# Kernel tuning notes

Hardware: AMD Instinct MI355X
Metric: run time of the kernel (lower is better)

The kernel has to match this reference:

```python
import jax, jax.numpy as jnp
import numpy as np

EPS_NORM = 1e-8
EPS_Q = 1e-5

def rmsnorm(x, g):
    var = jnp.mean(x * x, axis=-1, keepdims=True)
    return x * jax.lax.rsqrt(var + EPS_NORM) * g

def activation_quant(x):
    # per-token int8 absmax quantization
    scale = 127.0 / jnp.clip(jnp.max(jnp.abs(x), axis=-1, keepdims=True), EPS_Q, None)
    return jnp.clip(jnp.round(x * scale), -128.0, 127.0) / scale

def weight_quant(w):
    # per-tensor ternary absmean quantization
    scale = 1.0 / jnp.clip(jnp.mean(jnp.abs(w)), EPS_Q, None)
    return jnp.clip(jnp.round(w * scale), -1.0, 1.0) / scale

def ste(x, qfn):
    # straight-through estimator: forward quantized, backward identity
    return x + jax.lax.stop_gradient(qfn(x) - x)

def bitlinear(x, w, g):
    h = rmsnorm(x, g)
    hq = ste(h, activation_quant)
    wq = ste(w, weight_quant)
    return jnp.einsum('bsh,oh->bso', hq, wq)

def setup_inputs() -> dict:
    key = jax.random.key(0)
    k1, k2, k3 = jax.random.split(key, 3)
    B, S, H = 2, 2048, 2048
    I = int(H * 4.0)  # intermediate_size = 8192
    x = jax.random.normal(k1, (B, S, H), dtype=jnp.float32)
    w_gate = jax.random.normal(k2, (2 * I, H), dtype=jnp.float32) * 0.02
    g_gate = jnp.ones((H,), dtype=jnp.float32)
    w_down = jax.random.normal(k3, (H, I), dtype=jnp.float32) * 0.02
    g_down = jnp.ones((I,), dtype=jnp.float32)
    return {"x": x, "w_gate": w_gate, "g_gate": g_gate, "w_down": w_down, "g_down": g_down}

def reference(x, w_gate, g_gate, w_down, g_down):
    y = bitlinear(x, w_gate, g_gate)        # [B,S,2I]
    gate, up = jnp.split(y, 2, axis=-1)     # each [B,S,I]
    z = bitlinear(jax.nn.silu(gate) * up, w_down, g_down)  # [B,S,H]
    return z
```

## Files before the change

### kernel.cpp

```cpp
#include <hip/hip_runtime.h>
#include <hip/hip_bf16.h>
#include <hip/hip_fp16.h>

#define DEVINL __device__ __forceinline__

typedef float f32x4 __attribute__((ext_vector_type(4)));
typedef int i32x4 __attribute__((ext_vector_type(4)));
typedef unsigned int u32x4 __attribute__((ext_vector_type(4)));
typedef unsigned int u32x2 __attribute__((ext_vector_type(2)));

typedef __attribute__((address_space(1))) void void_g;
typedef __attribute__((address_space(3))) void void_l;

DEVINL void gload16(const void* g, void* l) {
  __builtin_amdgcn_global_load_lds((void_g*)g, (void_l*)l, 16, 0, 0);
}

DEVINL float wave_sum(float v) {
  #pragma unroll
  for (int o = 32; o > 0; o >>= 1) v += __shfl_down(v, o, 64);
  return v;
}
DEVINL float wave_max(float v) {
  #pragma unroll
  for (int o = 32; o > 0; o >>= 1) v = fmaxf(v, __shfl_down(v, o, 64));
  return v;
}

DEVINL unsigned int pack4(float a, float b, float c, float d) {
  return ((unsigned int)(unsigned char)(signed char)(int)a)
       | (((unsigned int)(unsigned char)(signed char)(int)b) << 8)
       | (((unsigned int)(unsigned char)(signed char)(int)c) << 16)
       | (((unsigned int)(unsigned char)(signed char)(int)d) << 24);
}

__global__ __launch_bounds__(256) void absum_kernel(const float* __restrict__ w,
                                                    long long nchunk, double* __restrict__ out) {
  long long stride = (long long)gridDim.x * 256;
  long long i = (long long)blockIdx.x * 256 + threadIdx.x;
  float s = 0.f;
  for (; i < nchunk; i += stride) {
    f32x4 v = ((const f32x4*)w)[i];
    s += fabsf(v[0]) + fabsf(v[1]) + fabsf(v[2]) + fabsf(v[3]);
  }
  s = wave_sum(s);
  __shared__ float red[4];
  int lane = threadIdx.x & 63, wv = threadIdx.x >> 6;
  if (lane == 0) red[wv] = s;
  __syncthreads();
  if (threadIdx.x == 0) atomicAdd(out, (double)(red[0] + red[1] + red[2] + red[3]));
}

__global__ __launch_bounds__(256) void quantw_kernel(const float* __restrict__ w,
                                                     signed char* __restrict__ tern,
                                                     long long nchunk,
                                                     const double* __restrict__ sum, double inv_n) {
  float scale = (float)(1.0 / fmax(*sum * inv_n, 1e-5));
  long long stride = (long long)gridDim.x * 256;
  long long i = (long long)blockIdx.x * 256 + threadIdx.x;
  for (; i < nchunk; i += stride) {
    f32x4 v0 = ((const f32x4*)w)[2 * i];
    f32x4 v1 = ((const f32x4*)w)[2 * i + 1];
    float t[8];
    #pragma unroll
    for (int k = 0; k < 4; k++) {
      t[k]     = fminf(fmaxf(rintf(v0[k] * scale), -1.f), 1.f);
      t[4 + k] = fminf(fmaxf(rintf(v1[k] * scale), -1.f), 1.f);
    }
    u32x2 o;
    o[0] = pack4(t[0], t[1], t[2], t[3]);
    o[1] = pack4(t[4], t[5], t[6], t[7]);
    ((u32x2*)tern)[i] = o;
  }
}

__global__ __launch_bounds__(256) void actq1_kernel(const float* __restrict__ x,
                                                    const float* __restrict__ g,
                                                    signed char* __restrict__ q,
                                                    float* __restrict__ a) {
  int t = blockIdx.x, tid = threadIdx.x;
  int lane = tid & 63, wv = tid >> 6;
  __shared__ float redS[4], redM[4];

  const f32x4* xr = (const f32x4*)(x + (size_t)t * 2048);
  f32x4 v0 = xr[tid * 2], v1 = xr[tid * 2 + 1];
  float ssq = 0.f;
  #pragma unroll
  for (int k = 0; k < 4; k++) ssq += v0[k] * v0[k] + v1[k] * v1[k];
  float ws_ = wave_sum(ssq);
  if (lane == 0) redS[wv] = ws_;
  __syncthreads();
  float tot = redS[0] + redS[1] + redS[2] + redS[3];
  float r = rsqrtf(tot / 2048.f + 1e-8f);

  f32x4 g0 = ((const f32x4*)g)[tid * 2], g1 = ((const f32x4*)g)[tid * 2 + 1];
  float h[8], amax = 0.f;
  #pragma unroll
  for (int k = 0; k < 4; k++) {
    h[k]     = v0[k] * r * g0[k];
    h[4 + k] = v1[k] * r * g1[k];
    amax = fmaxf(amax, fmaxf(fabsf(h[k]), fabsf(h[4 + k])));
  }
  float wm = wave_max(amax);
  if (lane == 0) redM[wv] = wm;
  __syncthreads();
  float am = fmaxf(fmaxf(fmaxf(redM[0], redM[1]), fmaxf(redM[2], redM[3])), 1e-5f);
  float scale = 127.f / am;

  float qv[8];
  #pragma unroll
  for (int k = 0; k < 8; k++) qv[k] = fminf(fmaxf(rintf(h[k] * scale), -128.f), 127.f);
  u32x2 o;
  o[0] = pack4(qv[0], qv[1], qv[2], qv[3]);
  o[1] = pack4(qv[4], qv[5], qv[6], qv[7]);
  ((u32x2*)(q + (size_t)t * 2048))[tid] = o;
  if (tid == 0) a[t] = am / 127.f;
}

__global__ __launch_bounds__(256) void silu_rms_q_kernel(const unsigned short* __restrict__ y,
                                                         const float* __restrict__ g,
                                                         signed char* __restrict__ q2,
                                                         float* __restrict__ a2) {
  int t = blockIdx.x, tid = threadIdx.x;
  int lane = tid & 63, wv = tid >> 6;
  __shared__ float redS[4], redM[4];
  const u32x4* gate = (const u32x4*)(y + (size_t)t * 16384);
  const u32x4* up   = (const u32x4*)(y + (size_t)t * 16384 + 8192);

  float v[32];
  float ssq = 0.f;
  #pragma unroll
  for (int b = 0; b < 4; b++) {
    u32x4 gr = gate[b * 256 + tid];
    u32x4 ur = up[b * 256 + tid];
    #pragma unroll
    for (int k = 0; k < 4; k++) {
      float g0 = __half2float(__ushort_as_half((unsigned short)(gr[k] & 0xFFFFu)));
      float g1 = __half2float(__ushort_as_half((unsigned short)(gr[k] >> 16)));
      float u0 = __half2float(__ushort_as_half((unsigned short)(ur[k] & 0xFFFFu)));
      float u1 = __half2float(__ushort_as_half((unsigned short)(ur[k] >> 16)));
      float v0 = g0 / (1.f + expf(-g0)) * u0;
      float v1 = g1 / (1.f + expf(-g1)) * u1;
      v[b * 8 + 2 * k] = v0;
      v[b * 8 + 2 * k + 1] = v1;
      ssq += v0 * v0 + v1 * v1;
    }
  }
  float ws_ = wave_sum(ssq);
  if (lane == 0) redS[wv] = ws_;
  __syncthreads();
  float tot = redS[0] + redS[1] + redS[2] + redS[3];
  float r = rsqrtf(tot / 8192.f + 1e-8f);

  float amax = 0.f;
  #pragma unroll
  for (int b = 0; b < 4; b++) {
    f32x4 ga = ((const f32x4*)g)[b * 512 + tid * 2];
    f32x4 gb = ((const f32x4*)g)[b * 512 + tid * 2 + 1];
    #pragma unroll
    for (int k = 0; k < 4; k++) {
      float h0 = v[b * 8 + k]     * r * ga[k];
      float h1 = v[b * 8 + 4 + k] * r * gb[k];
      v[b * 8 + k] = h0;
      v[b * 8 + 4 + k] = h1;
      amax = fmaxf(amax, fmaxf(fabsf(h0), fabsf(h1)));
    }
  }
  float wm = wave_max(amax);
  if (lane == 0) redM[wv] = wm;
  __syncthreads();
  float am = fmaxf(fmaxf(fmaxf(redM[0], redM[1]), fmaxf(redM[2], redM[3])), 1e-5f);
  float scale = 127.f / am;

  #pragma unroll
  for (int b = 0; b < 4; b++) {
    float qv[8];
    #pragma unroll
    for (int k = 0; k < 8; k++)
      qv[k] = fminf(fmaxf(rintf(v[b * 8 + k] * scale), -128.f), 127.f);
    u32x2 o;
    o[0] = pack4(qv[0], qv[1], qv[2], qv[3]);
    o[1] = pack4(qv[4], qv[5], qv[6], qv[7]);
    ((u32x2*)(q2 + (size_t)t * 8192))[b * 256 + tid] = o;
  }
  if (tid == 0) a2[t] = am / 127.f;
}

template <int OUT_MODE>
__global__ __launch_bounds__(256) void gemm_i8_kernel(const signed char* __restrict__ A,
                                                      const signed char* __restrict__ B,
                                                      void* __restrict__ Cv,
                                                      int M, int N, int K,
                                                      const float* __restrict__ rowscale,
                                                      const double* __restrict__ wsum, double inv_n) {
  __shared__ signed char As[8192];
  __shared__ signed char Bs[8192];
  const int tid = threadIdx.x;
  const int lane = tid & 63;
  const int wv = tid >> 6;
  const int wm = wv >> 1, wn = wv & 1;
  const int m0 = blockIdx.y * 128;
  const int n0 = blockIdx.x * 128;

  const int rr = tid >> 2;
  const int cc = (tid & 3) * 16;
  const signed char* Ag0 = A + (size_t)(m0 + rr) * K + cc;
  const signed char* Ag1 = A + (size_t)(m0 + 64 + rr) * K + cc;
  const signed char* Bg0 = B + (size_t)(n0 + rr) * K + cc;
  const signed char* Bg1 = B + (size_t)(n0 + 64 + rr) * K + cc;
  signed char* lA0 = &As[tid * 16];
  signed char* lA1 = &As[4096 + tid * 16];
  signed char* lB0 = &Bs[tid * 16];
  signed char* lB1 = &Bs[4096 + tid * 16];

  i32x4 acc[4][4] = {};

  const int fr = (lane & 15);
  const int kof = (lane >> 4) * 16;

  for (int k0 = 0; k0 < K; k0 += 64) {
    gload16(Ag0 + k0, lA0);
    gload16(Ag1 + k0, lA1);
    gload16(Bg0 + k0, lB0);
    gload16(Bg1 + k0, lB1);
    __syncthreads();
    i32x4 af[4], bfr[4];
    #pragma unroll
    for (int i = 0; i < 4; i++)
      af[i] = *(const i32x4*)&As[(wm * 64 + i * 16 + fr) * 64 + kof];
    #pragma unroll
    for (int j = 0; j < 4; j++)
      bfr[j] = *(const i32x4*)&Bs[(wn * 64 + j * 16 + fr) * 64 + kof];
    #pragma unroll
    for (int i = 0; i < 4; i++)
      #pragma unroll
      for (int j = 0; j < 4; j++)
        acc[i][j] = __builtin_amdgcn_mfma_i32_16x16x64_i8(af[i], bfr[j], acc[i][j], 0, 0, 0);
    __syncthreads();
  }

  float sw = (float)fmax(*wsum * inv_n, 1e-5);
  const int q = lane >> 4;
  const int cbase = n0 + wn * 64 + (lane & 15);
  #pragma unroll
  for (int i = 0; i < 4; i++) {
    int rowb = m0 + wm * 64 + i * 16 + q * 4;
    #pragma unroll
    for (int r = 0; r < 4; r++) {
      float sc = rowscale[rowb + r] * sw;
      size_t off = (size_t)(rowb + r) * N + cbase;
      #pragma unroll
      for (int j = 0; j < 4; j++) {
        float vv = (float)acc[i][j][r] * sc;
        if (OUT_MODE == 0) ((unsigned short*)Cv)[off + j * 16] = __half_as_ushort(__float2half(vv));
        else               ((float*)Cv)[off + j * 16] = vv;
      }
    }
  }
}

extern "C" void kernel_launch(void* const* d_in, const int* in_sizes, int n_in,
                              void* d_out, int out_size, void* d_ws, size_t ws_size,
                              hipStream_t stream) {
  const float* x      = (const float*)d_in[0];
  const float* w_gate = (const float*)d_in[1];
  const float* g_gate = (const float*)d_in[2];
  const float* w_down = (const float*)d_in[3];
  const float* g_down = (const float*)d_in[4];
  float* out = (float*)d_out;

  char* ws = (char*)d_ws;
  double* sums = (double*)ws;
  float* a1 = (float*)(ws + 4096);
  float* a2 = (float*)(ws + 20480);
  const size_t MB = 1024 * 1024;
  signed char* tern_g = (signed char*)(ws + 65536);
  signed char* q2     = tern_g;
  signed char* tern_d = (signed char*)(ws + 65536 + 32 * MB);
  signed char* q1     = (signed char*)(ws + 65536 + 48 * MB);
  unsigned short* yh  = (unsigned short*)(ws + 65536 + 56 * MB);

  hipMemsetAsync(sums, 0, 16, stream);
  absum_kernel<<<2048, 256, 0, stream>>>(w_gate, 33554432LL / 4, sums + 0);
  absum_kernel<<<1024, 256, 0, stream>>>(w_down, 16777216LL / 4, sums + 1);
  quantw_kernel<<<4096, 256, 0, stream>>>(w_gate, tern_g, 33554432LL / 8, sums + 0, 1.0 / 33554432.0);
  quantw_kernel<<<2048, 256, 0, stream>>>(w_down, tern_d, 16777216LL / 8, sums + 1, 1.0 / 16777216.0);
  actq1_kernel<<<4096, 256, 0, stream>>>(x, g_gate, q1, a1);
  gemm_i8_kernel<0><<<dim3(128, 32), 256, 0, stream>>>(q1, tern_g, yh, 4096, 16384, 2048,
                                                       a1, sums + 0, 1.0 / 33554432.0);
  silu_rms_q_kernel<<<4096, 256, 0, stream>>>(yh, g_down, q2, a2);
  gemm_i8_kernel<1><<<dim3(16, 32), 256, 0, stream>>>(q2, tern_d, out, 4096, 2048, 8192,
                                                      a2, sums + 1, 1.0 / 16777216.0);
}
```

Before: 663.2 us.

## Add 256x256-tile int8 GEMM with double-buffered LDS pipeline for gate projection

Adds a new int8 MFMA GEMM kernel with 256x256 output tiles, 512 threads and a 128 KB double-buffered LDS ring filled by direct global-to-LDS loads. Each K step is split into four phases that interleave MFMA work with async loads of the next tile, using barriers, raised wave priority during the MFMAs and an XOR swizzle to avoid LDS bank conflicts. Blocks are remapped across 8 groups for better cache locality. It replaces the first (gate/up) GEMM, aiming for more operand reuse and overlap of loads with compute. The large LDS footprint and heavy register use limit occupancy.

Measured after the change: 617.5 us. 6.9% less time.

```diff
diff --git a/kernel.cpp b/kernel.cpp
--- a/kernel.cpp
+++ b/kernel.cpp
@@ -259,6 +259,140 @@
   }
 }
 
+
+#define RD16(P, off) (*(const i32x4*)((P) + (off)))
+#define MFMA_I8(a, b, c) __builtin_amdgcn_mfma_i32_16x16x64_i8((a), (b), (c), 0, 0, 0)
+#define VM2 asm volatile("s_waitcnt vmcnt(2)" ::: "memory");
+#define VM0 asm volatile("s_waitcnt vmcnt(0)" ::: "memory");
+#define VMNONE
+
+#define PHASE(ks, h, DOB, STAGE, WAITV) { \
+  const int colb_ = ((((ks) << 6) | sq) ^ sfx);   \
+  const int ab_ = arow0 + (h) * 8192 + colb_; \
+  i32x4 fa0 = RD16(Ac, ab_); \
+  i32x4 fa1 = RD16(Ac, ab_ + 2048); \
+  i32x4 fa2 = RD16(Ac, ab_ + 4096); \
+  i32x4 fa3 = RD16(Ac, ab_ + 6144); \
+  if (DOB) { \
+    const int bb_ = brow0 + colb_; \
+    fb0 = RD16(Bc, bb_); \
+    fb1 = RD16(Bc, bb_ + 2048); \
+    fb2 = RD16(Bc, bb_ + 4096); \
+    fb3 = RD16(Bc, bb_ + 6144); \
+  } \
+  STAGE; \
+  __builtin_amdgcn_s_barrier(); \
+  asm volatile("s_waitcnt lgkmcnt(0)" ::: "memory"); \
+  __builtin_amdgcn_s_setprio(1); \
+  acc[(h) * 4 + 0][0] = MFMA_I8(fa0, fb0, acc[(h) * 4 + 0][0]); \
+  acc[(h) * 4 + 0][1] = MFMA_I8(fa0, fb1, acc[(h) * 4 + 0][1]); \
+  acc[(h) * 4 + 0][2] = MFMA_I8(fa0, fb2, acc[(h) * 4 + 0][2]); \
+  acc[(h) * 4 + 0][3] = MFMA_I8(fa0, fb3, acc[(h) * 4 + 0][3]); \
+  acc[(h) * 4 + 1][0] = MFMA_I8(fa1, fb0, acc[(h) * 4 + 1][0]); \
+  acc[(h) * 4 + 1][1] = MFMA_I8(fa1, fb1, acc[(h) * 4 + 1][1]); \
+  acc[(h) * 4 + 1][2] = MFMA_I8(fa1, fb2, acc[(h) * 4 + 1][2]); \
+  acc[(h) * 4 + 1][3] = MFMA_I8(fa1, fb3, acc[(h) * 4 + 1][3]); \
+  acc[(h) * 4 + 2][0] = MFMA_I8(fa2, fb0, acc[(h) * 4 + 2][0]); \
+  acc[(h) * 4 + 2][1] = MFMA_I8(fa2, fb1, acc[(h) * 4 + 2][1]); \
+  acc[(h) * 4 + 2][2] = MFMA_I8(fa2, fb2, acc[(h) * 4 + 2][2]); \
+  acc[(h) * 4 + 2][3] = MFMA_I8(fa2, fb3, acc[(h) * 4 + 2][3]); \
+  acc[(h) * 4 + 3][0] = MFMA_I8(fa3, fb0, acc[(h) * 4 + 3][0]); \
+  acc[(h) * 4 + 3][1] = MFMA_I8(fa3, fb1, acc[(h) * 4 + 3][1]); \
+  acc[(h) * 4 + 3][2] = MFMA_I8(fa3, fb2, acc[(h) * 4 + 3][2]); \
+  acc[(h) * 4 + 3][3] = MFMA_I8(fa3, fb3, acc[(h) * 4 + 3][3]); \
+  __builtin_amdgcn_s_setprio(0); \
+  WAITV \
+  __builtin_amdgcn_s_barrier(); }
+
+__global__ __launch_bounds__(512, 2) void gemm256_i8_kernel(
+    const signed char* __restrict__ A, const signed char* __restrict__ B,
+    unsigned short* __restrict__ C, int M, int N, int K,
+    const float* __restrict__ rowscale, const double* __restrict__ wsum, double inv_n) {
+  __shared__ __align__(16) signed char lds[131072];
+  const int tid = threadIdx.x;
+  const int lane = tid & 63;
+  const int wid = tid >> 6;
+  const int wr = wid >> 2;
+  const int wc = wid & 3;
+
+  const int nbn = N >> 8;
+  const int b = blockIdx.x;
+  const int cpx = gridDim.x >> 3;
+  const int sb = (b & 7) * cpx + (b >> 3);
+  const int m0 = (sb / nbn) << 8;
+  const int n0 = (sb % nbn) << 8;
+
+  const int fr = lane & 15;
+  const int sq = (lane >> 4) << 4;
+  const int sfx = (fr & 7) << 4;
+  const int arow0 = (wr * 128 + fr) * 128;
+  const int brow0 = (wc * 64 + fr) * 128;
+
+  const int rr = tid >> 3;
+  const int co = (((tid & 7) ^ (rr & 7)) << 4);
+  const signed char* gA = A + (size_t)(m0 + rr) * K + co;
+  const signed char* gB = B + (size_t)(n0 + rr) * K + co;
+  const size_t g64 = (size_t)64 * K;
+
+  i32x4 acc[8][4] = {};
+  i32x4 fb0, fb1, fb2, fb3;
+  const int NT = K >> 7;
+
+  {
+    signed char* Ad = lds + tid * 16;
+    signed char* Bd = Ad + 32768;
+    gload16(gB,           Bd);
+    gload16(gB + g64,     Bd + 8192);
+    gload16(gB + 2 * g64, Bd + 16384);
+    gload16(gB + 3 * g64, Bd + 24576);
+    gload16(gA,           Ad);
+    gload16(gA + 2 * g64, Ad + 16384);
+    gload16(gA + g64,     Ad + 8192);
+    gload16(gA + 3 * g64, Ad + 24576);
+    VM2
+    __builtin_amdgcn_s_barrier();
+  }
+
+  for (int t = 0; t < NT - 1; ++t) {
+    const signed char* Ac = lds + ((t & 1) << 16);
+    const signed char* Bc = Ac + 32768;
+    signed char* Ad = lds + (((t & 1) ^ 1) << 16) + tid * 16;
+    signed char* Bd = Ad + 32768;
+    const signed char* gAt = gA + (size_t)(t + 1) * 128;
+    const signed char* gBt = gB + (size_t)(t + 1) * 128;
+
+    PHASE(0, 0, 1, gload16(gBt, Bd); gload16(gBt + g64, Bd + 8192), VM2)
+    PHASE(0, 1, 0, gload16(gBt + 2 * g64, Bd + 16384); gload16(gBt + 3 * g64, Bd + 24576), VM2)
+    PHASE(1, 0, 1, gload16(gAt, Ad); gload16(gAt + 2 * g64, Ad + 16384), VM2)
+    PHASE(1, 1, 0, gload16(gAt + g64, Ad + 8192); gload16(gAt + 3 * g64, Ad + 24576), VM2)
+  }
+
+  {
+    const signed char* Ac = lds + (((NT - 1) & 1) << 16);
+    const signed char* Bc = Ac + 32768;
+    PHASE(0, 0, 1, , VM0)
+    PHASE(0, 1, 0, , VMNONE)
+    PHASE(1, 0, 1, , VMNONE)
+    PHASE(1, 1, 0, , VMNONE)
+  }
+
+  float sw = (float)fmax(*wsum * inv_n, 1e-5);
+  const int qo = lane >> 4;
+  const int cb = n0 + wc * 64 + fr;
+  #pragma unroll
+  for (int ai = 0; ai < 8; ai++) {
+    const int rowb = m0 + wr * 128 + ai * 16 + qo * 4;
+    #pragma unroll
+    for (int r = 0; r < 4; r++) {
+      float sc = rowscale[rowb + r] * sw;
+      size_t off = (size_t)(rowb + r) * N + cb;
+      #pragma unroll
+      for (int n = 0; n < 4; n++)
+        C[off + n * 16] = __half_as_ushort(__float2half((float)acc[ai][n][r] * sc));
+    }
+  }
+}
+
 extern "C" void kernel_launch(void* const* d_in, const int* in_sizes, int n_in,
                               void* d_out, int out_size, void* d_ws, size_t ws_size,
                               hipStream_t stream) {
@@ -286,8 +420,8 @@
   quantw_kernel<<<4096, 256, 0, stream>>>(w_gate, tern_g, 33554432LL / 8, sums + 0, 1.0 / 33554432.0);
   quantw_kernel<<<2048, 256, 0, stream>>>(w_down, tern_d, 16777216LL / 8, sums + 1, 1.0 / 16777216.0);
   actq1_kernel<<<4096, 256, 0, stream>>>(x, g_gate, q1, a1);
-  gemm_i8_kernel<0><<<dim3(128, 32), 256, 0, stream>>>(q1, tern_g, yh, 4096, 16384, 2048,
-                                                       a1, sums + 0, 1.0 / 33554432.0);
+  gemm256_i8_kernel<<<1024, 512, 0, stream>>>(q1, tern_g, yh, 4096, 16384, 2048,
+                                              a1, sums + 0, 1.0 / 33554432.0);
   silu_rms_q_kernel<<<4096, 256, 0, stream>>>(yh, g_down, q2, a2);
   gemm_i8_kernel<1><<<dim3(16, 32), 256, 0, stream>>>(q2, tern_d, out, 4096, 2048, 8192,
                                                       a2, sums + 1, 1.0 / 16777216.0);
```

## Rewrite int8 GEMM with 256x256 tiles, LDS double buffering and swizzled layout

Applied to the files above, without the earlier changes.

Replaces the 128x128, 4-wave int8 GEMM with a 256x256 tile, 8-wave kernel using K-step 128. Global-to-LDS loads for the next tile are double buffered and interleaved with MFMA clusters under setprio. The LDS layout is XOR-swizzled to avoid bank conflicts, and block IDs are remapped across XCDs. The goal is more data reuse and hidden load latency, at the cost of 128KB LDS per block. The down GEMM launches only 128 blocks, which may underfill the GPU.

Result: faster. 595.0 us (-10.3%).

```diff
diff --git a/kernel.cpp b/kernel.cpp
--- a/kernel.cpp
+++ b/kernel.cpp
@@ -186,74 +186,141 @@
   if (tid == 0) a2[t] = am / 127.f;
 }
 
+
+#define RD16(P, off) (*(const i32x4*)((P) + (off)))
+#define MFMA_I8(a, b, c) __builtin_amdgcn_mfma_i32_16x16x64_i8((a), (b), (c), 0, 0, 0)
+#define VM0 asm volatile("s_waitcnt vmcnt(0)" ::: "memory");
+
+#define CB(ks) ((((ks) << 6) | sq) ^ sfx)
+#define RDA(d0_, d1_, d2_, d3_, h, ks) { const int o_ = arow0 + (h) * 8192 + CB(ks); \
+  d0_ = RD16(Ac, o_); d1_ = RD16(Ac, o_ + 2048); d2_ = RD16(Ac, o_ + 4096); d3_ = RD16(Ac, o_ + 6144); }
+#define RDB(d0_, d1_, d2_, d3_, ks) { const int o_ = brow0 + CB(ks); \
+  d0_ = RD16(Bc, o_); d1_ = RD16(Bc, o_ + 2048); d2_ = RD16(Bc, o_ + 4096); d3_ = RD16(Bc, o_ + 6144); }
+
+#define CL(h, A0_, A1_, A2_, A3_, B0_, B1_, B2_, B3_) \
+  __builtin_amdgcn_s_setprio(1); \
+  acc[(h)*4+0][0] = MFMA_I8(A0_, B0_, acc[(h)*4+0][0]); \
+  acc[(h)*4+0][1] = MFMA_I8(A0_, B1_, acc[(h)*4+0][1]); \
+  acc[(h)*4+0][2] = MFMA_I8(A0_, B2_, acc[(h)*4+0][2]); \
+  acc[(h)*4+0][3] = MFMA_I8(A0_, B3_, acc[(h)*4+0][3]); \
+  acc[(h)*4+1][0] = MFMA_I8(A1_, B0_, acc[(h)*4+1][0]); \
+  acc[(h)*4+1][1] = MFMA_I8(A1_, B1_, acc[(h)*4+1][1]); \
+  acc[(h)*4+1][2] = MFMA_I8(A1_, B2_, acc[(h)*4+1][2]); \
+  acc[(h)*4+1][3] = MFMA_I8(A1_, B3_, acc[(h)*4+1][3]); \
+  acc[(h)*4+2][0] = MFMA_I8(A2_, B0_, acc[(h)*4+2][0]); \
+  acc[(h)*4+2][1] = MFMA_I8(A2_, B1_, acc[(h)*4+2][1]); \
+  acc[(h)*4+2][2] = MFMA_I8(A2_, B2_, acc[(h)*4+2][2]); \
+  acc[(h)*4+2][3] = MFMA_I8(A2_, B3_, acc[(h)*4+2][3]); \
+  acc[(h)*4+3][0] = MFMA_I8(A3_, B0_, acc[(h)*4+3][0]); \
+  acc[(h)*4+3][1] = MFMA_I8(A3_, B1_, acc[(h)*4+3][1]); \
+  acc[(h)*4+3][2] = MFMA_I8(A3_, B2_, acc[(h)*4+3][2]); \
+  acc[(h)*4+3][3] = MFMA_I8(A3_, B3_, acc[(h)*4+3][3]); \
+  __builtin_amdgcn_s_setprio(0);
+
+#define TILE_BODY(S1, S2, S3) { \
+  i32x4 a0, a1, a2, a3, b0, b1, b2, b3, c0, c1, c2, c3, d0, d1, d2, d3; \
+  RDA(a0, a1, a2, a3, 0, 0)             \
+  RDB(b0, b1, b2, b3, 0)                \
+  S1 \
+  RDA(c0, c1, c2, c3, 1, 0)             \
+  CL(0, a0, a1, a2, a3, b0, b1, b2, b3)               \
+  RDA(d0, d1, d2, d3, 0, 1)             \
+  RDB(a0, a1, a2, a3, 1)                \
+  S2 \
+  CL(1, c0, c1, c2, c3, b0, b1, b2, b3)               \
+  RDA(b0, b1, b2, b3, 1, 1)             \
+  S3 \
+  CL(0, d0, d1, d2, d3, a0, a1, a2, a3)               \
+  CL(1, b0, b1, b2, b3, a0, a1, a2, a3)               \
+}
+
 template <int OUT_MODE>
-__global__ __launch_bounds__(256) void gemm_i8_kernel(const signed char* __restrict__ A,
-                                                      const signed char* __restrict__ B,
-                                                      void* __restrict__ Cv,
-                                                      int M, int N, int K,
-                                                      const float* __restrict__ rowscale,
-                                                      const double* __restrict__ wsum, double inv_n) {
-  __shared__ signed char As[8192];
-  __shared__ signed char Bs[8192];
+__global__ __launch_bounds__(512, 2) void gemm256_i8_kernel(
+    const signed char* __restrict__ A, const signed char* __restrict__ B,
+    void* __restrict__ Cv, int M, int N, int K,
+    const float* __restrict__ rowscale, const double* __restrict__ wsum, double inv_n) {
+  __shared__ __align__(16) signed char lds[131072];
   const int tid = threadIdx.x;
   const int lane = tid & 63;
-  const int wv = tid >> 6;
-  const int wm = wv >> 1, wn = wv & 1;
-  const int m0 = blockIdx.y * 128;
-  const int n0 = blockIdx.x * 128;
-
-  const int rr = tid >> 2;
-  const int cc = (tid & 3) * 16;
-  const signed char* Ag0 = A + (size_t)(m0 + rr) * K + cc;
-  const signed char* Ag1 = A + (size_t)(m0 + 64 + rr) * K + cc;
-  const signed char* Bg0 = B + (size_t)(n0 + rr) * K + cc;
-  const signed char* Bg1 = B + (size_t)(n0 + 64 + rr) * K + cc;
-  signed char* lA0 = &As[tid * 16];
-  signed char* lA1 = &As[4096 + tid * 16];
-  signed char* lB0 = &Bs[tid * 16];
-  signed char* lB1 = &Bs[4096 + tid * 16];
-
-  i32x4 acc[4][4] = {};
-
-  const int fr = (lane & 15);
-  const int kof = (lane >> 4) * 16;
-
-  for (int k0 = 0; k0 < K; k0 += 64) {
-    gload16(Ag0 + k0, lA0);
-    gload16(Ag1 + k0, lA1);
-    gload16(Bg0 + k0, lB0);
-    gload16(Bg1 + k0, lB1);
-    __syncthreads();
-    i32x4 af[4], bfr[4];
-    #pragma unroll
-    for (int i = 0; i < 4; i++)
-      af[i] = *(const i32x4*)&As[(wm * 64 + i * 16 + fr) * 64 + kof];
-    #pragma unroll
-    for (int j = 0; j < 4; j++)
-      bfr[j] = *(const i32x4*)&Bs[(wn * 64 + j * 16 + fr) * 64 + kof];
-    #pragma unroll
-    for (int i = 0; i < 4; i++)
-      #pragma unroll
-      for (int j = 0; j < 4; j++)
-        acc[i][j] = __builtin_amdgcn_mfma_i32_16x16x64_i8(af[i], bfr[j], acc[i][j], 0, 0, 0);
-    __syncthreads();
+  const int wid = tid >> 6;
+  const int wr = wid >> 2;
+  const int wc = wid & 3;
+
+  const int nbn = N >> 8;
+  const int b = blockIdx.x;
+  const int cpx = gridDim.x >> 3;
+  const int sb = (b & 7) * cpx + (b >> 3);
+  const int m0 = (sb / nbn) << 8;
+  const int n0 = (sb % nbn) << 8;
+
+  const int fr = lane & 15;
+  const int sq = (lane >> 4) << 4;
+  const int sfx = (fr & 7) << 4;
+  const int arow0 = (wr * 128 + fr) * 128;
+  const int brow0 = (wc * 64 + fr) * 128;
+
+  const int rr = tid >> 3;
+  const int co = (((tid & 7) ^ (rr & 7)) << 4);
+  const signed char* gA = A + (size_t)(m0 + rr) * K + co;
+  const signed char* gB = B + (size_t)(n0 + rr) * K + co;
+  const size_t g64 = (size_t)64 * K;
+
+  i32x4 acc[8][4] = {};
+  const int NT = K >> 7;
+
+  {
+    signed char* Ad = lds + tid * 16;
+    signed char* Bd = Ad + 32768;
+    gload16(gB,           Bd);
+    gload16(gB + g64,     Bd + 8192);
+    gload16(gB + 2 * g64, Bd + 16384);
+    gload16(gB + 3 * g64, Bd + 24576);
+    gload16(gA,           Ad);
+    gload16(gA + g64,     Ad + 8192);
+    gload16(gA + 2 * g64, Ad + 16384);
+    gload16(gA + 3 * g64, Ad + 24576);
+    VM0
+    __builtin_amdgcn_s_barrier();
+  }
+
+  for (int t = 0; t < NT - 1; ++t) {
+    const signed char* Ac = lds + ((t & 1) << 16);
+    const signed char* Bc = Ac + 32768;
+    signed char* Ad = lds + (((t & 1) ^ 1) << 16) + tid * 16;
+    signed char* Bd = Ad + 32768;
+    const signed char* gAt = gA + (size_t)(t + 1) * 128;
+    const signed char* gBt = gB + (size_t)(t + 1) * 128;
+
+    TILE_BODY(
+      gload16(gBt, Bd); gload16(gBt + g64, Bd + 8192); gload16(gBt + 2 * g64, Bd + 16384); ,
+      gload16(gBt + 3 * g64, Bd + 24576); gload16(gAt, Ad); gload16(gAt + 2 * g64, Ad + 16384); ,
+      gload16(gAt + g64, Ad + 8192); gload16(gAt + 3 * g64, Ad + 24576); )
+
+    VM0
+    __builtin_amdgcn_s_barrier();
+  }
+
+  {
+    const signed char* Ac = lds + (((NT - 1) & 1) << 16);
+    const signed char* Bc = Ac + 32768;
+    TILE_BODY(, , )
   }
 
   float sw = (float)fmax(*wsum * inv_n, 1e-5);
-  const int q = lane >> 4;
-  const int cbase = n0 + wn * 64 + (lane & 15);
-  #pragma unroll
-  for (int i = 0; i < 4; i++) {
-    int rowb = m0 + wm * 64 + i * 16 + q * 4;
+  const int qo = lane >> 4;
+  const int cb = n0 + wc * 64 + fr;
+  #pragma unroll
+  for (int ai = 0; ai < 8; ai++) {
+    const int rowb = m0 + wr * 128 + ai * 16 + qo * 4;
     #pragma unroll
     for (int r = 0; r < 4; r++) {
       float sc = rowscale[rowb + r] * sw;
-      size_t off = (size_t)(rowb + r) * N + cbase;
+      size_t off = (size_t)(rowb + r) * N + cb;
       #pragma unroll
-      for (int j = 0; j < 4; j++) {
-        float vv = (float)acc[i][j][r] * sc;
-        if (OUT_MODE == 0) ((unsigned short*)Cv)[off + j * 16] = __half_as_ushort(__float2half(vv));
-        else               ((float*)Cv)[off + j * 16] = vv;
+      for (int n = 0; n < 4; n++) {
+        float vv = (float)acc[ai][n][r] * sc;
+        if (OUT_MODE == 0) ((unsigned short*)Cv)[off + n * 16] = __half_as_ushort(__float2half(vv));
+        else               ((float*)Cv)[off + n * 16] = vv;
       }
     }
   }
@@ -286,9 +353,9 @@
   quantw_kernel<<<4096, 256, 0, stream>>>(w_gate, tern_g, 33554432LL / 8, sums + 0, 1.0 / 33554432.0);
   quantw_kernel<<<2048, 256, 0, stream>>>(w_down, tern_d, 16777216LL / 8, sums + 1, 1.0 / 16777216.0);
   actq1_kernel<<<4096, 256, 0, stream>>>(x, g_gate, q1, a1);
-  gemm_i8_kernel<0><<<dim3(128, 32), 256, 0, stream>>>(q1, tern_g, yh, 4096, 16384, 2048,
-                                                       a1, sums + 0, 1.0 / 33554432.0);
+  gemm256_i8_kernel<0><<<1024, 512, 0, stream>>>(q1, tern_g, yh, 4096, 16384, 2048,
+                                                 a1, sums + 0, 1.0 / 33554432.0);
   silu_rms_q_kernel<<<4096, 256, 0, stream>>>(yh, g_down, q2, a2);
-  gemm_i8_kernel<1><<<dim3(16, 32), 256, 0, stream>>>(q2, tern_d, out, 4096, 2048, 8192,
-                                                      a2, sums + 1, 1.0 / 16777216.0);
-}
+  gemm256_i8_kernel<1><<<128, 512, 0, stream>>>(q2, tern_d, out, 4096, 2048, 8192,
+                                                a2, sums + 1, 1.0 / 16777216.0);
+}
```
